# Kernel tuning notes

Hardware: AMD Instinct MI355X
Metric: run time of the kernel (lower is better)

Reference implementation:

```python
import jax, jax.numpy as jnp
import numpy as np

B_, H_, W_, DMODEL = 4, 56, 56, 96
DSTATE = 16
DIN = int(2.0 * DMODEL)      # d_inner = ssm_ratio * d_model
RANK = int(np.ceil(DMODEL / 16))  # dt_rank 'auto'
K = 4                         # 4 scan directions


def setup_inputs() -> dict:
    key = jax.random.key(0)
    ks = jax.random.split(key, 8)
    f = lambda k, shape, s=0.02: jax.random.normal(k, shape, jnp.float32) * s
    x = jax.random.normal(ks[0], (B_, H_, W_, DMODEL), jnp.float32)
    in_proj_w = f(ks[1], (2 * DIN, DMODEL))
    conv_w = f(ks[2], (DIN, 1, 3, 3), 0.1)          # depthwise 3x3
    conv_b = jnp.zeros((DIN,), jnp.float32)
    x_proj_weight = f(ks[3], (K, RANK + 2 * DSTATE, DIN))
    dt_projs_weight = f(ks[4], (K, DIN, RANK), 0.1)
    # dt bias = inverse-softplus of dt sampled log-uniform in [1e-3, 0.1]
    dt = jnp.exp(jax.random.uniform(ks[5], (K, DIN)) * (np.log(0.1) - np.log(0.001)) + np.log(0.001))
    dt_projs_bias = dt + jnp.log(-jnp.expm1(-dt))
    A_logs = jnp.log(jnp.tile(jnp.arange(1, DSTATE + 1, dtype=jnp.float32)[None, :], (K * DIN, 1)))
    Ds = jnp.ones((K * DIN,), jnp.float32)
    ln_gamma = jnp.ones((DIN,), jnp.float32)
    ln_beta = jnp.zeros((DIN,), jnp.float32)
    out_proj_w = f(ks[6], (DMODEL, DIN))
    return dict(x=x, in_proj_w=in_proj_w, conv_w=conv_w, conv_b=conv_b,
                x_proj_weight=x_proj_weight, dt_projs_weight=dt_projs_weight,
                dt_projs_bias=dt_projs_bias, A_logs=A_logs, Ds=Ds,
                ln_gamma=ln_gamma, ln_beta=ln_beta, out_proj_w=out_proj_w)


def _ss2d(x, in_proj_w, conv_w, conv_b, x_proj_weight, dt_projs_weight,
          dt_projs_bias, A_logs, Ds, ln_gamma, ln_beta, out_proj_w):
    B, H, W, _ = x.shape
    L, D, N = H * W, DIN, DSTATE
    # input projection, split into x and gate z
    xz = x @ in_proj_w.T                                   # [B,H,W,2D]
    xc, z = jnp.split(xz, 2, axis=-1)
    z = jax.nn.silu(z)
    # depthwise 3x3 conv (NCHW) + SiLU
    xc = xc.transpose(0, 3, 1, 2)                          # [B,D,H,W]
    xc = jax.lax.conv_general_dilated(
        xc, conv_w, (1, 1), 'SAME',
        dimension_numbers=('NCHW', 'OIHW', 'NCHW'),
        feature_group_count=D) + conv_b[None, :, None, None]
    xc = jax.nn.silu(xc)
    # 4-directional cross scan: HW, WH, and their reverses
    x_hw = xc.reshape(B, D, L)
    x_wh = xc.transpose(0, 1, 3, 2).reshape(B, D, L)
    x2 = jnp.stack([x_hw, x_wh], axis=1)                   # [B,2,D,L]
    xs = jnp.concatenate([x2, jnp.flip(x2, axis=-1)], axis=1)  # [B,K,D,L]
    # per-direction projections to (dt_rank, B, C)
    x_dbl = jnp.einsum('bkdl,kcd->bkcl', xs, x_proj_weight)
    dts, Bs, Cs = jnp.split(x_dbl, [RANK, RANK + N], axis=2)   # [B,K,R|N|N,L]
    dts = jnp.einsum('bkrl,kdr->bkdl', dts, dt_projs_weight)   # [B,K,D,L]
    A = -jnp.exp(A_logs).reshape(K, D, N)
    delta = jax.nn.softplus(dts + dt_projs_bias[None, :, :, None])  # [B,K,D,L]
    # selective state-space scan over L
    u_t = xs.transpose(3, 0, 1, 2)     # [L,B,K,D]
    d_t = delta.transpose(3, 0, 1, 2)  # [L,B,K,D]
    B_t = Bs.transpose(3, 0, 1, 2)     # [L,B,K,N]
    C_t = Cs.transpose(3, 0, 1, 2)     # [L,B,K,N]

    def step(h, inp):
        dt_, u_, b_, c_ = inp
        dA = jnp.exp(dt_[..., None] * A)                       # [B,K,D,N]
        h = dA * h + dt_[..., None] * b_[:, :, None, :] * u_[..., None]
        y = jnp.einsum('bkdn,bkn->bkd', h, c_)
        return h, y

    h0 = jnp.zeros((B, K, D, N), jnp.float32)
    _, ys = jax.lax.scan(step, h0, (d_t, u_t, B_t, C_t))       # ys: [L,B,K,D]
    out_y = ys.transpose(1, 2, 3, 0) + Ds.reshape(K, D)[None, :, :, None] * xs  # [B,K,D,L]
    # merge the 4 directions back into HW order
    inv_y = jnp.flip(out_y[:, 2:4], axis=-1)                   # [B,2,D,L]
    wh_y = out_y[:, 1].reshape(B, D, W, H).transpose(0, 1, 3, 2).reshape(B, D, L)
    invwh_y = inv_y[:, 1].reshape(B, D, W, H).transpose(0, 1, 3, 2).reshape(B, D, L)
    y = out_y[:, 0] + inv_y[:, 0] + wh_y + invwh_y             # [B,D,L]
    y = y.transpose(0, 2, 1)                                   # [B,L,D]
    mu = y.mean(-1, keepdims=True)
    var = y.var(-1, keepdims=True)
    y = (y - mu) * jax.lax.rsqrt(var + 1e-5) * ln_gamma + ln_beta
    y = y.reshape(B, H, W, D) * z
    return y @ out_proj_w.T                                    # [B,H,W,d_model]


def reference(x, in_proj_w, conv_w, conv_b, x_proj_weight, dt_projs_weight,
              dt_projs_bias, A_logs, Ds, ln_gamma, ln_beta, out_proj_w):
    return _ss2d(x, in_proj_w, conv_w, conv_b, x_proj_weight, dt_projs_weight,
                 dt_projs_bias, A_logs, Ds, ln_gamma, ln_beta, out_proj_w)
```

## Files before the change

kernel.cpp:

```cpp
#include <hip/hip_runtime.h>
#include <math.h>

typedef __attribute__((ext_vector_type(2))) float f32x2;
typedef unsigned short u16;

constexpr int BB  = 4;
constexpr int HH  = 56;
constexpr int WW  = 56;
constexpr int CM  = 96;
constexpr int DD  = 192;
constexpr int NS  = 16;
constexpr int KK  = 4;
constexpr int LL  = HH * WW;
constexpr int CH  = 32;
constexpr int NCH = LL / CH;
constexpr int GC  = 7;
constexpr int G   = NCH / GC;
constexpr int PNCH = LL / 64;
constexpr int XDS = 40;
constexpr int MR  = 16;
constexpr int YS  = 196;

static __device__ __forceinline__ float siluf(float x) {
  return x / (1.f + __expf(-x));
}
static __device__ __forceinline__ u16 f2bf(float x) {
  unsigned u = __float_as_uint(x);
  u += 0x7fffu + ((u >> 16) & 1u);
  return (u16)(u >> 16);
}
static __device__ __forceinline__ float bf2f(u16 h) {
  return __uint_as_float(((unsigned)h) << 16);
}
static __device__ __forceinline__ unsigned pack2bf(float a, float b) {
  return ((unsigned)f2bf(b) << 16) | f2bf(a);
}
static __device__ __forceinline__ f32x2 up2bf(unsigned v) {
  return (f32x2){__uint_as_float(v << 16),
                 __uint_as_float(v & 0xffff0000u)};
}
static __device__ __forceinline__ int xcd_swz(int orig, int q) {
  return (orig & 7) * q + (orig >> 3);
}

__global__ __launch_bounds__(256) void k_prep(
    const float* __restrict__ ipw, const float* __restrict__ xpw,
    const float* __restrict__ cw, float* __restrict__ wTi2,
    float* __restrict__ wtp2, float* __restrict__ wcT) {
  int idx = blockIdx.x * 256 + threadIdx.x;
  if (idx < 96 * 384) {
    int n = idx / 96, k96 = idx % 96;
    int y = n / 48, r = n % 48;
    int wid = r / 12, j = r % 12;
    wTi2[(((size_t)(y * 4 + wid) * 96) + k96) * 12 + j] = ipw[n * 96 + k96];
  }
  int j2 = idx - 96 * 384;
  if (j2 >= 0 && j2 < KK * DD * 40) {
    int k = j2 / (DD * 40);
    int r = j2 % (DD * 40);
    int d = r / 40, ci = r % 40;
    int cg = ci / 10, q = ci % 10;
    wtp2[(((size_t)(k * 4 + cg) * DD) + d) * 10 + q] =
        (ci < 38) ? xpw[((size_t)k * 38 + ci) * DD + d] : 0.f;
  }
  int j3 = idx - 96 * 384 - KK * DD * 40;
  if (j3 >= 0 && j3 < 9 * DD) {
    int j = j3 / DD, d = j3 % DD;
    wcT[j * DD + d] = cw[d * 9 + j];
  }
}

__global__ __launch_bounds__(256) void k_inproj(
    const float* __restrict__ x, const float* __restrict__ wTi2,
    u16* __restrict__ xc16, u16* __restrict__ z16) {
  __shared__ float a[64 * 97];
  const int tid = threadIdx.x;
  const int m0 = blockIdx.x * 64;
  const int y  = blockIdx.y;
  const float4* xv = (const float4*)(x + (size_t)m0 * 96);
#pragma unroll
  for (int i = 0; i < 6; ++i) {
    int idx = tid + i * 256;
    int m = idx / 24, q = idx % 24;
    float4 v = xv[idx];
    a[m * 97 + 4 * q + 0] = v.x; a[m * 97 + 4 * q + 1] = v.y;
    a[m * 97 + 4 * q + 2] = v.z; a[m * 97 + 4 * q + 3] = v.w;
  }
  __syncthreads();
  const int lane = tid & 63;
  const int wid = __builtin_amdgcn_readfirstlane(threadIdx.x >> 6);
  const float* wrow = wTi2 + ((size_t)(y * 4 + wid) * 96) * 12;
  float acc[12];
#pragma unroll
  for (int j = 0; j < 12; ++j) acc[j] = 0.f;
  const float* arow = a + lane * 97;
#pragma unroll 4
  for (int k = 0; k < 96; ++k) {
    float u = arow[k];
    const float* wr = wrow + k * 12;
#pragma unroll
    for (int j = 0; j < 12; ++j) acc[j] = fmaf(wr[j], u, acc[j]);
  }
  __syncthreads();
#pragma unroll
  for (int j = 0; j < 12; ++j) a[lane * 97 + wid * 12 + j] = acc[j];
  __syncthreads();
  const bool isz = (y >= 4);
  u16* dst = isz ? z16 : xc16;
  const int c0 = (y & 3) * 48;
#pragma unroll
  for (int i = 0; i < 3; ++i) {
    int idx = tid + i * 256;
    int m = idx / 12, q = idx % 12;
    float v0 = a[m * 97 + q * 4 + 0], v1 = a[m * 97 + q * 4 + 1];
    float v2 = a[m * 97 + q * 4 + 2], v3 = a[m * 97 + q * 4 + 3];
    if (isz) { v0 = siluf(v0); v1 = siluf(v1);
               v2 = siluf(v2); v3 = siluf(v3); }
    *(uint2*)(dst + (size_t)(m0 + m) * DD + c0 + q * 4) =
        make_uint2(pack2bf(v0, v1), pack2bf(v2, v3));
  }
}

__global__ __launch_bounds__(256) void k_conv(
    const u16* __restrict__ xc16, const float* __restrict__ wcT,
    const float* __restrict__ cb, u16* __restrict__ xhw16) {
  const int blk = xcd_swz(blockIdx.x, (BB * HH * (WW / 2) * DD / 256) / 8);
  const int idx = blk * 256 + threadIdx.x;
  const int d = idx % DD;
  int t = idx / DD;
  const int wp = t % (WW / 2);
  t /= (WW / 2);
  const int h = t % HH;
  const int b = t / HH;
  const int w = wp * 2;
  const u16* src = xc16 + (size_t)b * LL * DD + d;
  float in[3][4];
#pragma unroll
  for (int r = 0; r < 3; ++r) {
    int hh = h + r - 1;
    bool hv = (hh >= 0 && hh < HH);
#pragma unroll
    for (int c = 0; c < 4; ++c) {
      int ww2 = w + c - 1;
      in[r][c] = (hv && ww2 >= 0 && ww2 < WW)
                     ? bf2f(src[((size_t)hh * WW + ww2) * DD]) : 0.f;
    }
  }
  float wgt[9];
#pragma unroll
  for (int j = 0; j < 9; ++j) wgt[j] = wcT[j * DD + d];
  const float base = cb[d];
  float a0 = base, a1 = base;
#pragma unroll
  for (int r = 0; r < 3; ++r)
#pragma unroll
    for (int c = 0; c < 3; ++c) {
      a0 = fmaf(wgt[r * 3 + c], in[r][c],     a0);
      a1 = fmaf(wgt[r * 3 + c], in[r][c + 1], a1);
    }
  u16* dst = xhw16 + ((size_t)b * LL + (size_t)h * WW + w) * DD + d;
  dst[0]  = f2bf(siluf(a0));
  dst[DD] = f2bf(siluf(a1));
}

__global__ __launch_bounds__(256) void k_xdbl(
    const u16* __restrict__ xhw16, const float* __restrict__ wtp2,
    float* __restrict__ xdbl32) {
  const int blk = xcd_swz(blockIdx.x, (BB * KK * PNCH) / 8);
  const int b = blk / (KK * PNCH);
  const int k = (blk / PNCH) % KK;
  const int c = blk % PNCH;
  const int l0 = c * 64;
  const bool rev = (k >= 2);
  const int pos = threadIdx.x & 63;
  const int cg = __builtin_amdgcn_readfirstlane(threadIdx.x >> 6);
  int tg = l0 + pos;
  int lg = rev ? (LL - 1 - tg) : tg;
  int row = (k & 1) ? ((lg % HH) * WW + lg / HH) : lg;
  const u16* ur = xhw16 + (size_t)b * LL * DD + (size_t)row * DD;
  const float* wbase = wtp2 + (size_t)(k * 4 + cg) * DD * 10;
  float acc[10];
#pragma unroll
  for (int q = 0; q < 10; ++q) acc[q] = 0.f;
#pragma unroll 2
  for (int d8 = 0; d8 < 24; ++d8) {
    uint4 uv = *(const uint4*)(ur + d8 * 8);
    f32x2 u01 = up2bf(uv.x), u23 = up2bf(uv.y);
    f32x2 u45 = up2bf(uv.z), u67 = up2bf(uv.w);
    const float* w0 = wbase + (size_t)(d8 * 8) * 10;
#pragma unroll
    for (int q = 0; q < 10; ++q) acc[q] = fmaf(w0[q],      u01.x, acc[q]);
#pragma unroll
    for (int q = 0; q < 10; ++q) acc[q] = fmaf(w0[10 + q], u01.y, acc[q]);
#pragma unroll
    for (int q = 0; q < 10; ++q) acc[q] = fmaf(w0[20 + q], u23.x, acc[q]);
#pragma unroll
    for (int q = 0; q < 10; ++q) acc[q] = fmaf(w0[30 + q], u23.y, acc[q]);
#pragma unroll
    for (int q = 0; q < 10; ++q) acc[q] = fmaf(w0[40 + q], u45.x, acc[q]);
#pragma unroll
    for (int q = 0; q < 10; ++q) acc[q] = fmaf(w0[50 + q], u45.y, acc[q]);
#pragma unroll
    for (int q = 0; q < 10; ++q) acc[q] = fmaf(w0[60 + q], u67.x, acc[q]);
#pragma unroll
    for (int q = 0; q < 10; ++q) acc[q] = fmaf(w0[70 + q], u67.y, acc[q]);
  }
  float* dst = xdbl32 + ((size_t)(b * KK + k) * LL + l0 + pos) * XDS;
#pragma unroll
  for (int q = 0; q < 10; ++q) {
    int ci = cg * 10 + q;
    int col = ci + (ci >= 6 ? 2 : 0);
    dst[col] = acc[q];
  }
}

static __device__ __forceinline__ int row_init(int k, bool rev, int l0,
                                               int& hh, int& ww) {
  int tg = rev ? (LL - 1 - l0) : l0;
  if (k & 1) {
    hh = tg % HH;
    ww = tg / HH;
    return hh * WW + ww;
  }
  return tg;
}
static __device__ __forceinline__ int row_next(int k, bool rev, int row,
                                               int& hh, int& ww) {
  if (k & 1) {
    if (!rev) { if (++hh == HH) { hh = 0; ++ww; } }
    else      { if (--hh < 0) { hh = HH - 1; --ww; } }
    return hh * WW + ww;
  }
  return rev ? row - 1 : row + 1;
}

__global__ __launch_bounds__(192) void k_scanY(
    const u16* __restrict__ xhw16, const float* __restrict__ xdbl32,
    const float* __restrict__ dtw, const float* __restrict__ dtb,
    const float* __restrict__ Ds, float* __restrict__ Qc,
    u16* __restrict__ Sc16, u16* __restrict__ ylc16) {
  __shared__ __align__(16) float xsf[CH * XDS];
  const int blk = blockIdx.x;
  const int b = blk / (KK * NCH);
  const int k = (blk / NCH) % KK;
  const int c = blk % NCH;
  const int l0 = c * CH;
  const bool rev = (k >= 2);
  const int d = threadIdx.x;
  const int bk = b * KK + k;
  {
    const float4* src = (const float4*)(xdbl32 + ((size_t)bk * LL + l0) * XDS);
    float4* dl = (float4*)xsf;
    dl[d] = src[d];
    if (d < CH * XDS / 4 - 192) dl[d + 192] = src[d + 192];
  }
  unsigned up[CH / 2];
  {
    const u16* uplane = xhw16 + (size_t)b * LL * DD + d;
    int hh, ww;
    int row = row_init(k, rev, l0, hh, ww);
#pragma unroll
    for (int t2 = 0; t2 < CH / 2; ++t2) {
      unsigned lo = uplane[(size_t)row * DD];
      row = row_next(k, rev, row, hh, ww);
      unsigned hi = uplane[(size_t)row * DD];
      row = row_next(k, rev, row, hh, ww);
      up[t2] = lo | (hi << 16);
    }
  }
  float w2[6];
#pragma unroll
  for (int r = 0; r < 6; ++r) w2[r] = dtw[((size_t)k * DD + d) * 6 + r];
  const float bias = dtb[k * DD + d];
  const float dsd = Ds[k * DD + d];
  f32x2 h2[8];
#pragma unroll
  for (int m = 0; m < 8; ++m) h2[m] = (f32x2){0.f, 0.f};
  float sumd = 0.f;
  u16* ybase = ylc16 + ((size_t)bk * LL + l0) * DD + d;
  __syncthreads();
#pragma unroll
  for (int t = 0; t < CH; ++t) {
    const float* xr = xsf + t * XDS;
    float4 fd0 = *(const float4*)(xr);
    f32x2  fd1 = *(const f32x2*)(xr + 4);
    float4 b0 = *(const float4*)(xr + 8);
    float4 b1 = *(const float4*)(xr + 12);
    float4 b2 = *(const float4*)(xr + 16);
    float4 b3 = *(const float4*)(xr + 20);
    float4 c0 = *(const float4*)(xr + 24);
    float4 c1 = *(const float4*)(xr + 28);
    float4 c2 = *(const float4*)(xr + 32);
    float4 c3 = *(const float4*)(xr + 36);
    unsigned uu = up[t >> 1];
    float u = __uint_as_float((t & 1) ? (uu & 0xffff0000u) : (uu << 16));
    float draw = bias;
    draw = fmaf(w2[0], fd0.x, draw);
    draw = fmaf(w2[1], fd0.y, draw);
    draw = fmaf(w2[2], fd0.z, draw);
    draw = fmaf(w2[3], fd0.w, draw);
    draw = fmaf(w2[4], fd1.x, draw);
    draw = fmaf(w2[5], fd1.y, draw);
    float e = __expf(draw);
    float p = __builtin_amdgcn_rcpf(1.f + e);
    float delta = (draw < 15.f) ? -__logf(p) : draw;
    sumd += delta;
    float du = delta * u;
    f32x2 duv = {du, du};
    float ps = p * p;
    f32x2 pw = {p, ps};
    f32x2 q2 = {ps, ps};
    f32x2 yacc = {0.f, 0.f};
    f32x2 bp[8] = {{b0.x, b0.y}, {b0.z, b0.w}, {b1.x, b1.y}, {b1.z, b1.w},
                   {b2.x, b2.y}, {b2.z, b2.w}, {b3.x, b3.y}, {b3.z, b3.w}};
    f32x2 cp[8] = {{c0.x, c0.y}, {c0.z, c0.w}, {c1.x, c1.y}, {c1.z, c1.w},
                   {c2.x, c2.y}, {c2.z, c2.w}, {c3.x, c3.y}, {c3.z, c3.w}};
#pragma unroll
    for (int m = 0; m < 8; ++m) {
      h2[m] = pw * h2[m] + duv * bp[m];
      yacc = yacc + h2[m] * cp[m];
      pw = pw * q2;
    }
    ybase[(size_t)t * DD] = f2bf(fmaf(dsd, u, yacc.x + yacc.y));
  }
  size_t qi = ((size_t)bk * NCH + c) * DD + d;
  Qc[qi] = sumd;
  unsigned* sp = (unsigned*)(Sc16 + qi * 16);
#pragma unroll
  for (int m = 0; m < 8; ++m) sp[m] = pack2bf(h2[m].x, h2[m].y);
}

__global__ __launch_bounds__(256) void k_pfxA(
    const float* __restrict__ Qc, const u16* __restrict__ Sc16,
    u16* __restrict__ Ag16, u16* __restrict__ Sg16) {
  const int blk = xcd_swz(blockIdx.x, (BB * KK * G * DD * NS / 256) / 8);
  int flat = blk * 256 + threadIdx.x;
  int n = flat & 15;
  int d = (flat >> 4) % DD;
  int g = (flat / (NS * DD)) % G;
  int bk = flat / (NS * DD * G);
  const float en = -(float)(n + 1);
  const size_t c0 = (size_t)bk * NCH + (size_t)g * GC;
  float Ecur = 0.f, qp = 0.f;
#pragma unroll
  for (int i = 0; i < GC; ++i) {
    size_t ci = (c0 + i) * DD + d;
    float q = Qc[ci];
    float s = bf2f(Sc16[ci * 16 + n]);
    Ecur = fmaf(__expf(en * q), Ecur, s);
    qp += q;
  }
  size_t gi = (((size_t)bk * G + g) * DD + d) * NS + n;
  Ag16[gi] = f2bf(__expf(en * qp));
  Sg16[gi] = f2bf(Ecur);
}

__global__ __launch_bounds__(192) void k_correct(
    const float* __restrict__ xdbl32, const u16* __restrict__ Ag16,
    const u16* __restrict__ Sg16, const float* __restrict__ Qc,
    const u16* __restrict__ Sc16, const u16* __restrict__ ylc16,
    const float* __restrict__ dtw, const float* __restrict__ dtb,
    u16* __restrict__ y16) {
  __shared__ __align__(16) float xsf[CH * XDS];
  const int blk = xcd_swz(blockIdx.x, (BB * KK * NCH) / 8);
  const int b = blk / (KK * NCH);
  const int k = (blk / NCH) % KK;
  const int c = blk % NCH;
  const int g = c / GC;
  const int l0 = c * CH;
  const bool rev = (k >= 2);
  const int d = threadIdx.x;
  const int bk = b * KK + k;
  {
    const float4* src = (const float4*)(xdbl32 + ((size_t)bk * LL + l0) * XDS);
    float4* dl = (float4*)xsf;
    dl[d] = src[d];
    if (d < CH * XDS / 4 - 192) dl[d + 192] = src[d + 192];
  }
  float w2[6];
#pragma unroll
  for (int r = 0; r < 6; ++r) w2[r] = dtw[((size_t)k * DD + d) * 6 + r];
  const float bias = dtb[k * DD + d];
  f32x2 h2[8];
#pragma unroll
  for (int m = 0; m < 8; ++m) h2[m] = (f32x2){0.f, 0.f};
  for (int g2 = 0; g2 < g; ++g2) {
    size_t gi = (((size_t)bk * G + g2) * DD + d) * NS;
    const u16* ap = Ag16 + gi;
    const u16* spg = Sg16 + gi;
    uint4 a0 = *(const uint4*)ap;
    uint4 a1 = *(const uint4*)(ap + 8);
    uint4 s0 = *(const uint4*)spg;
    uint4 s1 = *(const uint4*)(spg + 8);
    f32x2 av[8] = {up2bf(a0.x), up2bf(a0.y), up2bf(a0.z), up2bf(a0.w),
                   up2bf(a1.x), up2bf(a1.y), up2bf(a1.z), up2bf(a1.w)};
    f32x2 sv[8] = {up2bf(s0.x), up2bf(s0.y), up2bf(s0.z), up2bf(s0.w),
                   up2bf(s1.x), up2bf(s1.y), up2bf(s1.z), up2bf(s1.w)};
#pragma unroll
    for (int m = 0; m < 8; ++m) h2[m] = av[m] * h2[m] + sv[m];
  }
  for (int i = g * GC; i < c; ++i) {
    size_t ci = ((size_t)bk * NCH + i) * DD + d;
    float r = __expf(-Qc[ci]);
    const u16* sp = Sc16 + ci * 16;
    uint4 s0 = *(const uint4*)sp;
    uint4 s1 = *(const uint4*)(sp + 8);
    f32x2 sv[8] = {up2bf(s0.x), up2bf(s0.y), up2bf(s0.z), up2bf(s0.w),
                   up2bf(s1.x), up2bf(s1.y), up2bf(s1.z), up2bf(s1.w)};
    float r2 = r * r;
    f32x2 pw = {r, r2};
    f32x2 q2 = {r2, r2};
#pragma unroll
    for (int m = 0; m < 8; ++m) {
      h2[m] = pw * h2[m] + sv[m];
      pw = pw * q2;
    }
  }
  const u16* ybase = ylc16 + ((size_t)bk * LL + l0) * DD + d;
  u16* yplane = y16 + (size_t)bk * LL * DD + d;
  int hh, ww;
  int row = row_init(k, rev, l0, hh, ww);
  float pe = 1.f;
  __syncthreads();
#pragma unroll
  for (int t = 0; t < CH; ++t) {
    const float* xr = xsf + t * XDS;
    float4 fd0 = *(const float4*)(xr);
    f32x2  fd1 = *(const f32x2*)(xr + 4);
    float4 c0 = *(const float4*)(xr + 24);
    float4 c1 = *(const float4*)(xr + 28);
    float4 c2 = *(const float4*)(xr + 32);
    float4 c3 = *(const float4*)(xr + 36);
    float yl = bf2f(ybase[(size_t)t * DD]);
    float draw = bias;
    draw = fmaf(w2[0], fd0.x, draw);
    draw = fmaf(w2[1], fd0.y, draw);
    draw = fmaf(w2[2], fd0.z, draw);
    draw = fmaf(w2[3], fd0.w, draw);
    draw = fmaf(w2[4], fd1.x, draw);
    draw = fmaf(w2[5], fd1.y, draw);
    float e = __expf(draw);
    float p = __builtin_amdgcn_rcpf(1.f + e);
    pe *= p;
    float p1 = pe;
    float ps = p1 * p1;
    f32x2 pw = {p1, ps};
    f32x2 q2 = {ps, ps};
    f32x2 yacc = {0.f, 0.f};
    f32x2 cp[8] = {{c0.x, c0.y}, {c0.z, c0.w}, {c1.x, c1.y}, {c1.z, c1.w},
                   {c2.x, c2.y}, {c2.z, c2.w}, {c3.x, c3.y}, {c3.z, c3.w}};
#pragma unroll
    for (int m = 0; m < 8; ++m) {
      yacc = yacc + (pw * h2[m]) * cp[m];
      pw = pw * q2;
    }
    yplane[(size_t)row * DD] = f2bf(yl + yacc.x + yacc.y);
    row = row_next(k, rev, row, hh, ww);
  }
}

__global__ __launch_bounds__(256) void k_merge_out(
    const u16* __restrict__ y16, const u16* __restrict__ z16,
    const float* __restrict__ gamma, const float* __restrict__ beta,
    const float* __restrict__ wo, float* __restrict__ out) {
  __shared__ float ym[MR][YS];
  __shared__ float ssum[MR][17];
  __shared__ float ssq[MR][17];
  __shared__ float stat[MR][2];
  const int tid = threadIdx.x;
  const int m0 = blockIdx.x * MR;
  const int b = m0 / LL;
  const int lb = m0 % LL;
  const u16* P = y16 + (size_t)b * KK * LL * DD;
  constexpr size_t PL = (size_t)LL * DD;
#pragma unroll
  for (int i = 0; i < MR * (DD / 2) / 256; ++i) {
    int idx = tid + i * 256;
    int row = idx / (DD / 2), pr = idx % (DD / 2);
    size_t base = (size_t)(lb + row) * DD + pr * 2;
    float s0 = 0.f, s1 = 0.f;
#pragma unroll
    for (int pl = 0; pl < 4; ++pl) {
      unsigned v = *(const unsigned*)(P + pl * PL + base);
      f32x2 vv = up2bf(v);
      s0 += vv.x; s1 += vv.y;
    }
    *(f32x2*)&ym[row][pr * 2] = (f32x2){s0, s1};
  }
  __syncthreads();
  {
    int r2 = tid & 15, os = tid >> 4;
    float s = 0.f, sq = 0.f;
#pragma unroll
    for (int i = 0; i < 12; ++i) {
      float v = ym[r2][os * 12 + i];
      s += v; sq = fmaf(v, v, sq);
    }
    ssum[r2][os] = s; ssq[r2][os] = sq;
  }
  __syncthreads();
  if (tid < MR) {
    float s = 0.f, sq = 0.f;
#pragma unroll
    for (int i = 0; i < 16; ++i) { s += ssum[tid][i]; sq += ssq[tid][i]; }
    float mean = s * (1.f / DD);
    float var = sq * (1.f / DD) - mean * mean;
    stat[tid][0] = mean;
    stat[tid][1] = rsqrtf(var + 1e-5f);
  }
  __syncthreads();
#pragma unroll
  for (int i = 0; i < MR * DD / 256; ++i) {
    int idx = tid + i * 256;
    int r2 = idx / DD, d = idx % DD;
    float v = (ym[r2][d] - stat[r2][0]) * stat[r2][1] * gamma[d] + beta[d];
    v *= bf2f(z16[(size_t)(m0 + r2) * DD + d]);
    ym[r2][d] = v;
  }
  __syncthreads();
  const int r0 = (tid & 7) * 2;
  const int os = tid >> 3;
  float acc0[3] = {}, acc1[3] = {};
  for (int d4 = 0; d4 < 48; ++d4) {
    float4 a0 = *(const float4*)&ym[r0][d4 * 4];
    float4 a1 = *(const float4*)&ym[r0 + 1][d4 * 4];
#pragma unroll
    for (int j = 0; j < 3; ++j) {
      const float4 w4 =
          *(const float4*)(wo + (size_t)(os * 3 + j) * DD + d4 * 4);
      acc0[j] = fmaf(w4.x, a0.x,
                fmaf(w4.y, a0.y, fmaf(w4.z, a0.z, fmaf(w4.w, a0.w, acc0[j]))));
      acc1[j] = fmaf(w4.x, a1.x,
                fmaf(w4.y, a1.y, fmaf(w4.z, a1.z, fmaf(w4.w, a1.w, acc1[j]))));
    }
  }
  __syncthreads();
#pragma unroll
  for (int j = 0; j < 3; ++j) {
    ym[r0][os * 3 + j] = acc0[j];
    ym[r0 + 1][os * 3 + j] = acc1[j];
  }
  __syncthreads();
  for (int idx = tid; idx < MR * (CM / 4); idx += 256) {
    int r2 = idx / (CM / 4), c4 = idx % (CM / 4);
    float4 v = *(const float4*)&ym[r2][c4 * 4];
    *(float4*)(out + (size_t)(m0 + r2) * CM + c4 * 4) = v;
  }
}

extern "C" void kernel_launch(void* const* d_in, const int* in_sizes, int n_in,
                              void* d_out, int out_size, void* d_ws,
                              size_t ws_size, hipStream_t stream) {
  (void)in_sizes; (void)n_in; (void)out_size; (void)ws_size;
  const float* x   = (const float*)d_in[0];
  const float* ipw = (const float*)d_in[1];
  const float* cw  = (const float*)d_in[2];
  const float* cb  = (const float*)d_in[3];
  const float* xpw = (const float*)d_in[4];
  const float* dtw = (const float*)d_in[5];
  const float* dtb = (const float*)d_in[6];
  const float* Ds  = (const float*)d_in[8];
  const float* gam = (const float*)d_in[9];
  const float* bet = (const float*)d_in[10];
  const float* wo  = (const float*)d_in[11];
  float* out = (float*)d_out;

  char* pb = (char*)d_ws;
  u16* z16   = (u16*)pb; pb += (size_t)BB * LL * DD * 2;
  u16* xc16  = (u16*)pb; pb += (size_t)BB * LL * DD * 2;
  u16* xhw16 = (u16*)pb; pb += (size_t)BB * LL * DD * 2;
  float* xdbl32 = (float*)pb; pb += (size_t)BB * KK * LL * XDS * 4;
  float* Qc  = (float*)pb; pb += (size_t)BB * KK * NCH * DD * 4;
  float* wTi2 = (float*)pb; pb += 96 * 384 * 4;
  float* wtp2 = (float*)pb; pb += KK * DD * 40 * 4;
  float* wcT = (float*)pb; pb += 9 * DD * 4;
  u16* Sc16 = (u16*)pb; pb += (size_t)BB * KK * NCH * DD * NS * 2;
  u16* Ag16 = (u16*)pb; pb += (size_t)BB * KK * G * DD * NS * 2;
  u16* Sg16 = (u16*)pb; pb += (size_t)BB * KK * G * DD * NS * 2;
  u16* ylc16 = (u16*)pb; pb += (size_t)BB * KK * LL * DD * 2;
  u16* y16  = (u16*)pb; pb += (size_t)BB * KK * LL * DD * 2;

  k_prep<<<dim3(272), 256, 0, stream>>>(ipw, xpw, cw, wTi2, wtp2, wcT);
  k_inproj<<<dim3(196, 8), 256, 0, stream>>>(x, wTi2, xc16, z16);
  k_conv<<<dim3(BB * HH * (WW / 2) * DD / 256), 256, 0, stream>>>(
      xc16, wcT, cb, xhw16);
  k_xdbl<<<dim3(BB * KK * PNCH), 256, 0, stream>>>(xhw16, wtp2, xdbl32);
  k_scanY<<<dim3(BB * KK * NCH), 192, 0, stream>>>(
      xhw16, xdbl32, dtw, dtb, Ds, Qc, Sc16, ylc16);
  k_pfxA<<<dim3(BB * KK * G * DD * NS / 256), 256, 0, stream>>>(
      Qc, Sc16, Ag16, Sg16);
  k_correct<<<dim3(BB * KK * NCH), 192, 0, stream>>>(
      xdbl32, Ag16, Sg16, Qc, Sc16, ylc16, dtw, dtb, y16);
  k_merge_out<<<dim3(BB * LL / MR), 256, 0, stream>>>(
      y16, z16, gam, bet, wo, out);
}
```

Baseline: 216.2 us.

## Pair forward and reverse scan directions per block to share u loads

Each scan block now handles a forward direction and its reverse counterpart on the mirrored chunk, so the gathered u values from xhw16 are loaded once and used by both directions. This halves the grid and the strided u gathers. In exchange each thread carries two state sets and twice the registers and LDS, which may lower occupancy. The two independent recurrences are interleaved and could add ILP.

```diff
diff --git a/kernel.cpp b/kernel.cpp
--- a/kernel.cpp
+++ b/kernel.cpp
@@ -239,95 +239,160 @@
     const float* __restrict__ dtw, const float* __restrict__ dtb,
     const float* __restrict__ Ds, float* __restrict__ Qc,
     u16* __restrict__ Sc16, u16* __restrict__ ylc16) {
-  __shared__ __align__(16) float xsf[CH * XDS];
+  __shared__ __align__(16) float xsf0[CH * XDS];
+  __shared__ __align__(16) float xsf1[CH * XDS];
   const int blk = blockIdx.x;
-  const int b = blk / (KK * NCH);
-  const int k = (blk / NCH) % KK;
+  const int b = blk / (2 * NCH);
+  const int kp = (blk / NCH) % 2;
   const int c = blk % NCH;
+  const int k0 = kp;
+  const int k1 = kp + 2;
+  const int cpr = NCH - 1 - c;
   const int l0 = c * CH;
-  const bool rev = (k >= 2);
   const int d = threadIdx.x;
-  const int bk = b * KK + k;
+  const int bk0 = b * KK + k0;
+  const int bk1 = b * KK + k1;
   {
-    const float4* src = (const float4*)(xdbl32 + ((size_t)bk * LL + l0) * XDS);
-    float4* dl = (float4*)xsf;
-    dl[d] = src[d];
-    if (d < CH * XDS / 4 - 192) dl[d + 192] = src[d + 192];
+    const float4* s0 =
+        (const float4*)(xdbl32 + ((size_t)bk0 * LL + l0) * XDS);
+    const float4* s1 =
+        (const float4*)(xdbl32 + ((size_t)bk1 * LL + (size_t)cpr * CH) * XDS);
+    float4* d0 = (float4*)xsf0;
+    float4* d1 = (float4*)xsf1;
+    for (int i = d; i < CH * XDS / 4; i += 192) { d0[i] = s0[i]; d1[i] = s1[i]; }
   }
   unsigned up[CH / 2];
   {
     const u16* uplane = xhw16 + (size_t)b * LL * DD + d;
     int hh, ww;
-    int row = row_init(k, rev, l0, hh, ww);
+    int row = row_init(k0, false, l0, hh, ww);
 #pragma unroll
     for (int t2 = 0; t2 < CH / 2; ++t2) {
       unsigned lo = uplane[(size_t)row * DD];
-      row = row_next(k, rev, row, hh, ww);
+      row = row_next(k0, false, row, hh, ww);
       unsigned hi = uplane[(size_t)row * DD];
-      row = row_next(k, rev, row, hh, ww);
+      row = row_next(k0, false, row, hh, ww);
       up[t2] = lo | (hi << 16);
     }
   }
-  float w2[6];
-#pragma unroll
-  for (int r = 0; r < 6; ++r) w2[r] = dtw[((size_t)k * DD + d) * 6 + r];
-  const float bias = dtb[k * DD + d];
-  const float dsd = Ds[k * DD + d];
-  f32x2 h2[8];
-#pragma unroll
-  for (int m = 0; m < 8; ++m) h2[m] = (f32x2){0.f, 0.f};
-  float sumd = 0.f;
-  u16* ybase = ylc16 + ((size_t)bk * LL + l0) * DD + d;
+  float w2a[6], w2b[6];
+#pragma unroll
+  for (int r = 0; r < 6; ++r) {
+    w2a[r] = dtw[((size_t)k0 * DD + d) * 6 + r];
+    w2b[r] = dtw[((size_t)k1 * DD + d) * 6 + r];
+  }
+  const float biasa = dtb[k0 * DD + d];
+  const float biasb = dtb[k1 * DD + d];
+  const float dsda = Ds[k0 * DD + d];
+  const float dsdb = Ds[k1 * DD + d];
+  f32x2 ha[8], hb[8];
+#pragma unroll
+  for (int m = 0; m < 8; ++m) { ha[m] = (f32x2){0.f, 0.f};
+                                hb[m] = (f32x2){0.f, 0.f}; }
+  float sumda = 0.f, sumdb = 0.f;
+  u16* ybase0 = ylc16 + ((size_t)bk0 * LL + l0) * DD + d;
+  u16* ybase1 = ylc16 + ((size_t)bk1 * LL + (size_t)cpr * CH) * DD + d;
   __syncthreads();
 #pragma unroll
   for (int t = 0; t < CH; ++t) {
-    const float* xr = xsf + t * XDS;
-    float4 fd0 = *(const float4*)(xr);
-    f32x2  fd1 = *(const f32x2*)(xr + 4);
-    float4 b0 = *(const float4*)(xr + 8);
-    float4 b1 = *(const float4*)(xr + 12);
-    float4 b2 = *(const float4*)(xr + 16);
-    float4 b3 = *(const float4*)(xr + 20);
-    float4 c0 = *(const float4*)(xr + 24);
-    float4 c1 = *(const float4*)(xr + 28);
-    float4 c2 = *(const float4*)(xr + 32);
-    float4 c3 = *(const float4*)(xr + 36);
-    unsigned uu = up[t >> 1];
-    float u = __uint_as_float((t & 1) ? (uu & 0xffff0000u) : (uu << 16));
-    float draw = bias;
-    draw = fmaf(w2[0], fd0.x, draw);
-    draw = fmaf(w2[1], fd0.y, draw);
-    draw = fmaf(w2[2], fd0.z, draw);
-    draw = fmaf(w2[3], fd0.w, draw);
-    draw = fmaf(w2[4], fd1.x, draw);
-    draw = fmaf(w2[5], fd1.y, draw);
-    float e = __expf(draw);
-    float p = __builtin_amdgcn_rcpf(1.f + e);
-    float delta = (draw < 15.f) ? -__logf(p) : draw;
-    sumd += delta;
-    float du = delta * u;
-    f32x2 duv = {du, du};
-    float ps = p * p;
-    f32x2 pw = {p, ps};
-    f32x2 q2 = {ps, ps};
-    f32x2 yacc = {0.f, 0.f};
-    f32x2 bp[8] = {{b0.x, b0.y}, {b0.z, b0.w}, {b1.x, b1.y}, {b1.z, b1.w},
-                   {b2.x, b2.y}, {b2.z, b2.w}, {b3.x, b3.y}, {b3.z, b3.w}};
-    f32x2 cp[8] = {{c0.x, c0.y}, {c0.z, c0.w}, {c1.x, c1.y}, {c1.z, c1.w},
-                   {c2.x, c2.y}, {c2.z, c2.w}, {c3.x, c3.y}, {c3.z, c3.w}};
-#pragma unroll
-    for (int m = 0; m < 8; ++m) {
-      h2[m] = pw * h2[m] + duv * bp[m];
-      yacc = yacc + h2[m] * cp[m];
-      pw = pw * q2;
-    }
-    ybase[(size_t)t * DD] = f2bf(fmaf(dsd, u, yacc.x + yacc.y));
-  }
-  size_t qi = ((size_t)bk * NCH + c) * DD + d;
-  Qc[qi] = sumd;
-  unsigned* sp = (unsigned*)(Sc16 + qi * 16);
-#pragma unroll
-  for (int m = 0; m < 8; ++m) sp[m] = pack2bf(h2[m].x, h2[m].y);
+    {
+      const float* xr = xsf0 + t * XDS;
+      float4 fd0 = *(const float4*)(xr);
+      f32x2  fd1 = *(const f32x2*)(xr + 4);
+      float4 b0 = *(const float4*)(xr + 8);
+      float4 b1 = *(const float4*)(xr + 12);
+      float4 b2 = *(const float4*)(xr + 16);
+      float4 b3 = *(const float4*)(xr + 20);
+      float4 c0 = *(const float4*)(xr + 24);
+      float4 c1 = *(const float4*)(xr + 28);
+      float4 c2 = *(const float4*)(xr + 32);
+      float4 c3 = *(const float4*)(xr + 36);
+      unsigned uu = up[t >> 1];
+      float u = __uint_as_float((t & 1) ? (uu & 0xffff0000u) : (uu << 16));
+      float draw = biasa;
+      draw = fmaf(w2a[0], fd0.x, draw);
+      draw = fmaf(w2a[1], fd0.y, draw);
+      draw = fmaf(w2a[2], fd0.z, draw);
+      draw = fmaf(w2a[3], fd0.w, draw);
+      draw = fmaf(w2a[4], fd1.x, draw);
+      draw = fmaf(w2a[5], fd1.y, draw);
+      float e = __expf(draw);
+      float p = __builtin_amdgcn_rcpf(1.f + e);
+      float delta = (draw < 15.f) ? -__logf(p) : draw;
+      sumda += delta;
+      float du = delta * u;
+      f32x2 duv = {du, du};
+      float ps = p * p;
+      f32x2 pw = {p, ps};
+      f32x2 q2 = {ps, ps};
+      f32x2 yacc = {0.f, 0.f};
+      f32x2 bp[8] = {{b0.x, b0.y}, {b0.z, b0.w}, {b1.x, b1.y}, {b1.z, b1.w},
+                     {b2.x, b2.y}, {b2.z, b2.w}, {b3.x, b3.y}, {b3.z, b3.w}};
+      f32x2 cp[8] = {{c0.x, c0.y}, {c0.z, c0.w}, {c1.x, c1.y}, {c1.z, c1.w},
+                     {c2.x, c2.y}, {c2.z, c2.w}, {c3.x, c3.y}, {c3.z, c3.w}};
+#pragma unroll
+      for (int m = 0; m < 8; ++m) {
+        ha[m] = pw * ha[m] + duv * bp[m];
+        yacc = yacc + ha[m] * cp[m];
+        pw = pw * q2;
+      }
+      ybase0[(size_t)t * DD] = f2bf(fmaf(dsda, u, yacc.x + yacc.y));
+    }
+    {
+      const float* xr = xsf1 + t * XDS;
+      float4 fd0 = *(const float4*)(xr);
+      f32x2  fd1 = *(const f32x2*)(xr + 4);
+      float4 b0 = *(const float4*)(xr + 8);
+      float4 b1 = *(const float4*)(xr + 12);
+      float4 b2 = *(const float4*)(xr + 16);
+      float4 b3 = *(const float4*)(xr + 20);
+      float4 c0 = *(const float4*)(xr + 24);
+      float4 c1 = *(const float4*)(xr + 28);
+      float4 c2 = *(const float4*)(xr + 32);
+      float4 c3 = *(const float4*)(xr + 36);
+      unsigned uu = up[(CH - 1 - t) >> 1];
+      float u = __uint_as_float(((CH - 1 - t) & 1) ? (uu & 0xffff0000u)
+                                                   : (uu << 16));
+      float draw = biasb;
+      draw = fmaf(w2b[0], fd0.x, draw);
+      draw = fmaf(w2b[1], fd0.y, draw);
+      draw = fmaf(w2b[2], fd0.z, draw);
+      draw = fmaf(w2b[3], fd0.w, draw);
+      draw = fmaf(w2b[4], fd1.x, draw);
+      draw = fmaf(w2b[5], fd1.y, draw);
+      float e = __expf(draw);
+      float p = __builtin_amdgcn_rcpf(1.f + e);
+      float delta = (draw < 15.f) ? -__logf(p) : draw;
+      sumdb += delta;
+      float du = delta * u;
+      f32x2 duv = {du, du};
+      float ps = p * p;
+      f32x2 pw = {p, ps};
+      f32x2 q2 = {ps, ps};
+      f32x2 yacc = {0.f, 0.f};
+      f32x2 bp[8] = {{b0.x, b0.y}, {b0.z, b0.w}, {b1.x, b1.y}, {b1.z, b1.w},
+                     {b2.x, b2.y}, {b2.z, b2.w}, {b3.x, b3.y}, {b3.z, b3.w}};
+      f32x2 cp[8] = {{c0.x, c0.y}, {c0.z, c0.w}, {c1.x, c1.y}, {c1.z, c1.w},
+                     {c2.x, c2.y}, {c2.z, c2.w}, {c3.x, c3.y}, {c3.z, c3.w}};
+#pragma unroll
+      for (int m = 0; m < 8; ++m) {
+        hb[m] = pw * hb[m] + duv * bp[m];
+        yacc = yacc + hb[m] * cp[m];
+        pw = pw * q2;
+      }
+      ybase1[(size_t)t * DD] = f2bf(fmaf(dsdb, u, yacc.x + yacc.y));
+    }
+  }
+  size_t qi0 = ((size_t)bk0 * NCH + c) * DD + d;
+  Qc[qi0] = sumda;
+  unsigned* sp0 = (unsigned*)(Sc16 + qi0 * 16);
+#pragma unroll
+  for (int m = 0; m < 8; ++m) sp0[m] = pack2bf(ha[m].x, ha[m].y);
+  size_t qi1 = ((size_t)bk1 * NCH + cpr) * DD + d;
+  Qc[qi1] = sumdb;
+  unsigned* sp1 = (unsigned*)(Sc16 + qi1 * 16);
+#pragma unroll
+  for (int m = 0; m < 8; ++m) sp1[m] = pack2bf(hb[m].x, hb[m].y);
 }
 
 __global__ __launch_bounds__(256) void k_pfxA(
@@ -585,7 +650,7 @@
   k_conv<<<dim3(BB * HH * (WW / 2) * DD / 256), 256, 0, stream>>>(
       xc16, wcT, cb, xhw16);
   k_xdbl<<<dim3(BB * KK * PNCH), 256, 0, stream>>>(xhw16, wtp2, xdbl32);
-  k_scanY<<<dim3(BB * KK * NCH), 192, 0, stream>>>(
+  k_scanY<<<dim3(BB * 2 * NCH), 192, 0, stream>>>(
       xhw16, xdbl32, dtw, dtb, Ds, Qc, Sc16, ylc16);
   k_pfxA<<<dim3(BB * KK * G * DD * NS / 256), 256, 0, stream>>>(
       Qc, Sc16, Ag16, Sg16);
```

After: 217.7 us. No clear change (+0.7%).
